# Kernel optimization log

Hardware: AMD Instinct MI355X
Metric: run time of the kernel (lower is better)

Reference implementation:

```python
import math
import jax, jax.numpy as jnp
import numpy as np

B, T, D, H, FACTOR = 8, 4096, 1024, 16, 5
DH = D // H


def setup_inputs() -> dict:
    key = jax.random.key(0)
    ks = jax.random.split(key, 7)
    u = max(1, min(int(FACTOR * math.log(T + 1)), T))  # = 41
    s = 1.0 / np.sqrt(D).astype(np.float32)
    x = jax.random.normal(ks[0], (B, T, D), jnp.float32)
    Wq = jax.random.normal(ks[1], (D, D), jnp.float32) * s
    Wk = jax.random.normal(ks[2], (D, D), jnp.float32) * s
    Wv = jax.random.normal(ks[3], (D, D), jnp.float32) * s
    Wo = jax.random.normal(ks[4], (D, D), jnp.float32) * s
    bo = jax.random.normal(ks[5], (D,), jnp.float32) * 0.01
    # unique indices, mirroring torch.randperm(T)[:u]
    idx = jax.random.permutation(ks[6], T)[:u].astype(jnp.int32)
    return {"x": x, "Wq": Wq, "Wk": Wk, "Wv": Wv, "Wo": Wo, "bo": bo, "idx": idx}


def reference(x, Wq, Wk, Wv, Wo, bo, idx):
    Bx, Tx, Dx = x.shape
    scale = 1.0 / np.sqrt(DH).astype(np.float32)

    def proj(W):  # torch Linear: x @ W.T, then split heads -> [B,H,T,Dh]
        return (x @ W.T).reshape(Bx, Tx, H, DH).transpose(0, 2, 1, 3)

    Q = proj(Wq)
    K = proj(Wk)
    V = proj(Wv)

    Qs = Q[:, :, idx, :]                                   # [B,H,u,Dh] gather
    scores = jnp.einsum('bhud,bhtd->bhut', Qs, K) * scale  # [B,H,u,T]
    attn = jax.nn.softmax(scores, axis=-1)
    ctx = jnp.einsum('bhut,bhtd->bhud', attn, V)           # [B,H,u,Dh]

    # mean over the u sampled positions fills non-sampled slots
    out = jnp.broadcast_to(ctx.mean(axis=2, keepdims=True), (Bx, H, Tx, DH))
    out = out.at[:, :, idx, :].set(ctx)                    # scatter ctx back

    y = out.transpose(0, 2, 1, 3).reshape(Bx, Tx, Dx)
    return y @ Wo.T + bo
```

## Files before the change

kernel.cpp:

```cpp
#include <hip/hip_runtime.h>
#include <hip/hip_bf16.h>

#define B_  8
#define T_  4096
#define D_  1024
#define H_  16
#define DH_ 64
#define NC_ 4

typedef __bf16 bf8 __attribute__((ext_vector_type(8)));
typedef float f32x4 __attribute__((ext_vector_type(4)));

__device__ __forceinline__ unsigned short f2bf_rn(float f) {
    unsigned u = __float_as_uint(f);
    unsigned r = (u + 0x7FFF + ((u >> 16) & 1)) >> 16;
    return (unsigned short)r;
}

__device__ __forceinline__ void async_load16(const void* gp, void* lp) {
    __builtin_amdgcn_global_load_lds(
        (const __attribute__((address_space(1))) unsigned*)(gp),
        (__attribute__((address_space(3))) unsigned*)(lp), 16, 0, 0);
}


__global__ void k_sel(const int* __restrict__ idx, int* __restrict__ sel, int U) {
    for (int t = threadIdx.x; t < T_; t += 256) sel[t] = 0;
    __syncthreads();
    if (threadIdx.x < U) sel[idx[threadIdx.x]] = threadIdx.x + 1;
}

__global__ void k_gather(const float* __restrict__ x, const int* __restrict__ idx,
                         float* __restrict__ xs, int U) {
    int bi = blockIdx.x;
    int b = bi / U, i = bi - b * U;
    int t = idx[i];
    const float4* src = (const float4*)(x + ((size_t)(b * T_ + t)) * D_);
    float4* dst = (float4*)(xs + (size_t)bi * D_);
    dst[threadIdx.x] = src[threadIdx.x];
}

__global__ void k_cvt_flat(const float* __restrict__ src, short* __restrict__ dst) {
    size_t i = ((size_t)blockIdx.x * 256 + threadIdx.x) * 8;
    float4 a = *(const float4*)(src + i);
    float4 b = *(const float4*)(src + i + 4);
    short4 s0, s1;
    s0.x = (short)f2bf_rn(a.x); s0.y = (short)f2bf_rn(a.y);
    s0.z = (short)f2bf_rn(a.z); s0.w = (short)f2bf_rn(a.w);
    s1.x = (short)f2bf_rn(b.x); s1.y = (short)f2bf_rn(b.y);
    s1.z = (short)f2bf_rn(b.z); s1.w = (short)f2bf_rn(b.w);
    *(short4*)(dst + i) = s0;
    *(short4*)(dst + i + 4) = s1;
}

__global__ __launch_bounds__(256) void k_proj(const float* __restrict__ A,
                                              const float* __restrict__ W,
                                              const float* __restrict__ bias,
                                              float* __restrict__ C, int M) {
    __shared__ float As[32][64 + 4];
    __shared__ float Bs[32][64 + 4];
    int m0 = blockIdx.x * 64, n0 = blockIdx.y * 64;
    int tid = threadIdx.x;
    int lr = tid >> 3;
    int lc = (tid & 7) * 4;
    int ty = tid >> 4, tx = tid & 15;
    float acc[4][4] = {{0.f}};
    for (int k0 = 0; k0 < D_; k0 += 32) {
#pragma unroll
        for (int half = 0; half < 2; ++half) {
            int r = lr + half * 32;
            int gm = m0 + r;
            float4 v = make_float4(0.f, 0.f, 0.f, 0.f);
            if (gm < M) v = *(const float4*)(A + (size_t)gm * D_ + k0 + lc);
            As[lc + 0][r] = v.x; As[lc + 1][r] = v.y; As[lc + 2][r] = v.z; As[lc + 3][r] = v.w;
            int gn = n0 + r;
            float4 w = *(const float4*)(W + (size_t)gn * D_ + k0 + lc);
            Bs[lc + 0][r] = w.x; Bs[lc + 1][r] = w.y; Bs[lc + 2][r] = w.z; Bs[lc + 3][r] = w.w;
        }
        __syncthreads();
#pragma unroll
        for (int kk = 0; kk < 32; ++kk) {
            float4 a = *(const float4*)&As[kk][ty * 4];
            float4 bb = *(const float4*)&Bs[kk][tx * 4];
            acc[0][0] += a.x * bb.x; acc[0][1] += a.x * bb.y; acc[0][2] += a.x * bb.z; acc[0][3] += a.x * bb.w;
            acc[1][0] += a.y * bb.x; acc[1][1] += a.y * bb.y; acc[1][2] += a.y * bb.z; acc[1][3] += a.y * bb.w;
            acc[2][0] += a.z * bb.x; acc[2][1] += a.z * bb.y; acc[2][2] += a.z * bb.z; acc[2][3] += a.z * bb.w;
            acc[3][0] += a.w * bb.x; acc[3][1] += a.w * bb.y; acc[3][2] += a.w * bb.z; acc[3][3] += a.w * bb.w;
        }
        __syncthreads();
    }
#pragma unroll
    for (int i = 0; i < 4; ++i) {
        int gm = m0 + ty * 4 + i;
        if (gm < M) {
            int gn = n0 + tx * 4;
            float4 v = make_float4(acc[i][0], acc[i][1], acc[i][2], acc[i][3]);
            if (bias) {
                v.x += bias[gn + 0]; v.y += bias[gn + 1];
                v.z += bias[gn + 2]; v.w += bias[gn + 3];
            }
            *(float4*)(C + (size_t)gm * D_ + gn) = v;
        }
    }
}

__global__ __launch_bounds__(256) void k_qth(const float* __restrict__ Qs,
                                             const float* __restrict__ Wk,
                                             short* __restrict__ Qtb, int U, int MP) {
    __shared__ float As[32][64 + 4];
    __shared__ float Bs[32][64 + 4];
    int h = blockIdx.z;
    int m0 = blockIdx.x * 64, n0 = blockIdx.y * 64;
    int BU = B_ * U;
    int tid = threadIdx.x;
    int lr = tid >> 3, lc = (tid & 7) * 4;
    int ty = tid >> 4, tx = tid & 15;
    float acc[4][4] = {{0.f}};
    for (int k0 = 0; k0 < DH_; k0 += 32) {
#pragma unroll
        for (int half = 0; half < 2; ++half) {
            int r = lr + half * 32;
            int gm = m0 + r;
            float4 v = make_float4(0.f, 0.f, 0.f, 0.f);
            if (gm < BU) v = *(const float4*)(Qs + (size_t)gm * D_ + h * DH_ + k0 + lc);
            As[lc + 0][r] = v.x; As[lc + 1][r] = v.y; As[lc + 2][r] = v.z; As[lc + 3][r] = v.w;
            int kr = (tid >> 4) + half * 16;
            int nc = (tid & 15) * 4;
            float4 w = *(const float4*)(Wk + ((size_t)(h * DH_ + k0 + kr)) * D_ + n0 + nc);
            *(float4*)&Bs[kr][nc] = w;
        }
        __syncthreads();
#pragma unroll
        for (int kk = 0; kk < 32; ++kk) {
            float4 a = *(const float4*)&As[kk][ty * 4];
            float4 bb = *(const float4*)&Bs[kk][tx * 4];
            acc[0][0] += a.x * bb.x; acc[0][1] += a.x * bb.y; acc[0][2] += a.x * bb.z; acc[0][3] += a.x * bb.w;
            acc[1][0] += a.y * bb.x; acc[1][1] += a.y * bb.y; acc[1][2] += a.y * bb.z; acc[1][3] += a.y * bb.w;
            acc[2][0] += a.z * bb.x; acc[2][1] += a.z * bb.y; acc[2][2] += a.z * bb.z; acc[2][3] += a.z * bb.w;
            acc[3][0] += a.w * bb.x; acc[3][1] += a.w * bb.y; acc[3][2] += a.w * bb.z; acc[3][3] += a.w * bb.w;
        }
        __syncthreads();
    }
#pragma unroll
    for (int i = 0; i < 4; ++i) {
        int gm = m0 + ty * 4 + i;
        if (gm < BU) {
            int b = gm / U, ii = gm - b * U;
            short4 s;
            s.x = (short)f2bf_rn(0.125f * acc[i][0]);
            s.y = (short)f2bf_rn(0.125f * acc[i][1]);
            s.z = (short)f2bf_rn(0.125f * acc[i][2]);
            s.w = (short)f2bf_rn(0.125f * acc[i][3]);
            *(short4*)(Qtb + ((size_t)b * MP + h * U + ii) * D_ + n0 + tx * 4) = s;
        }
    }
}

#define GEMM_NT 16

__device__ __forceinline__ void stage64(const short* __restrict__ Ag,
                                        const short* __restrict__ Bg,
                                        short* lA, short* lB, int kt, int tid) {
#pragma unroll
    for (int i = 0; i < 4; ++i) {
        int li = i * 512 + tid;
        int row = li >> 3, sl = li & 7;
        int off = row * D_ + kt + ((sl ^ (row & 7)) << 3);
        async_load16(Ag + off, lA + li * 8);
        async_load16(Bg + off, lB + li * 8);
    }
}

__device__ __forceinline__ bf8 lds_frag(const short* l, int R, int slot) {
    return *(const bf8*)(l + R * 64 + (((slot) ^ (R & 7)) << 3));
}

__device__ __forceinline__ void gemm256_core(const short* __restrict__ Ag,
                                             const short* __restrict__ Bg,
                                             short* lA0, short* lB0,
                                             f32x4 (&acc)[8][4]) {
    int tid = threadIdx.x;
    int lane = tid & 63, w = tid >> 6;
    int wr = w >> 2, wc = w & 3;
    int ln = lane & 15, q = lane >> 4;
#pragma unroll
    for (int mi = 0; mi < 8; ++mi)
#pragma unroll
        for (int ni = 0; ni < 4; ++ni)
            acc[mi][ni] = (f32x4){0.f, 0.f, 0.f, 0.f};

    stage64(Ag, Bg, lA0, lB0, 0, tid);
    stage64(Ag, Bg, lA0 + 16384, lB0 + 16384, 64, tid);

#pragma unroll 1
    for (int t = 0; t < GEMM_NT; ++t) {
        const int p = t & 1;
        short* lA = lA0 + p * 16384;
        short* lB = lB0 + p * 16384;
        if (t < GEMM_NT - 1) asm volatile("s_waitcnt vmcnt(8)" ::: "memory");
        else                 asm volatile("s_waitcnt vmcnt(0)" ::: "memory");
        __builtin_amdgcn_s_barrier();

        bf8 bfrag[4][2], afrag[4][2];
#pragma unroll
        for (int ni = 0; ni < 4; ++ni)
#pragma unroll
            for (int kh = 0; kh < 2; ++kh)
                bfrag[ni][kh] = lds_frag(lB, wc * 64 + ni * 16 + ln, kh * 4 + q);
#pragma unroll
        for (int mi = 0; mi < 4; ++mi)
#pragma unroll
            for (int kh = 0; kh < 2; ++kh)
                afrag[mi][kh] = lds_frag(lA, wr * 128 + mi * 16 + ln, kh * 4 + q);
        __builtin_amdgcn_s_setprio(1);
#pragma unroll
        for (int kh = 0; kh < 2; ++kh)
#pragma unroll
            for (int mi = 0; mi < 4; ++mi)
#pragma unroll
                for (int ni = 0; ni < 4; ++ni)
                    acc[mi][ni] = __builtin_amdgcn_mfma_f32_16x16x32_bf16(
                        afrag[mi][kh], bfrag[ni][kh], acc[mi][ni], 0, 0, 0);
        __builtin_amdgcn_s_setprio(0);
#pragma unroll
        for (int mi = 0; mi < 4; ++mi)
#pragma unroll
            for (int kh = 0; kh < 2; ++kh)
                afrag[mi][kh] = lds_frag(lA, wr * 128 + 64 + mi * 16 + ln, kh * 4 + q);
        __builtin_amdgcn_s_setprio(1);
#pragma unroll
        for (int kh = 0; kh < 2; ++kh)
#pragma unroll
            for (int mi = 0; mi < 4; ++mi)
#pragma unroll
                for (int ni = 0; ni < 4; ++ni)
                    acc[4 + mi][ni] = __builtin_amdgcn_mfma_f32_16x16x32_bf16(
                        afrag[mi][kh], bfrag[ni][kh], acc[4 + mi][ni], 0, 0, 0);
        __builtin_amdgcn_s_setprio(0);
        asm volatile("" ::: "memory");
        __builtin_amdgcn_s_barrier();
        if (t + 2 < GEMM_NT)
            stage64(Ag, Bg, lA, lB, (t + 2) * 64, tid);
    }
}

__global__ __launch_bounds__(512, 2) void k_gemm(const short* __restrict__ Qtb,
                                                 const short* __restrict__ xb,
                                                 const short* __restrict__ Wvb,
                                                 short* __restrict__ attnb,
                                                 short* __restrict__ Vt, int MP) {
    __shared__ short lAB[4][16384];
    int bid = blockIdx.x;
    int cpx = gridDim.x >> 3;
    int lg = (bid & 7) * cpx + (bid >> 3);
    int tid = threadIdx.x;
    int lane = tid & 63, w = tid >> 6;
    int wr = w >> 2, wc = w & 3;
    int ln = lane & 15, q = lane >> 4;
    f32x4 acc[8][4];

    if (lg < 512) {
        int mt = lg >> 2, nt = lg & 3;
        gemm256_core(xb + (size_t)mt * 256 * D_, Wvb + (size_t)nt * 256 * D_,
                     &lAB[0][0], &lAB[2][0], acc);
        int h = nt * 4 + wc;
        int b = mt >> 4;
        int tIn = (mt & 15) * 256 + wr * 128;
        const int PITCH = 136;
        short* ep = &lAB[0][0] + w * 2304;
        size_t vbase = ((size_t)(b * H_ + h) * DH_) * T_;
#pragma unroll
        for (int ni = 0; ni < 4; ++ni) {
#pragma unroll
            for (int mi = 0; mi < 8; ++mi) {
                short4 s;
                s.x = (short)f2bf_rn(acc[mi][ni][0]);
                s.y = (short)f2bf_rn(acc[mi][ni][1]);
                s.z = (short)f2bf_rn(acc[mi][ni][2]);
                s.w = (short)f2bf_rn(acc[mi][ni][3]);
                *(short4*)(ep + ln * PITCH + mi * 16 + q * 4) = s;
            }
            __syncthreads();
#pragma unroll
            for (int it = 0; it < 2; ++it) {
                int dhl = it * 8 + (lane >> 3);
                int seg = lane & 7;
                bf8 v0 = *(const bf8*)(ep + dhl * PITCH + seg * 8);
                bf8 v1 = *(const bf8*)(ep + dhl * PITCH + (seg + 8) * 8);
                int dh = ni * 16 + dhl;
                *(bf8*)(Vt + vbase + (size_t)dh * T_ + tIn + seg * 8) = v0;
                *(bf8*)(Vt + vbase + (size_t)dh * T_ + tIn + 64 + seg * 8) = v1;
            }
            __syncthreads();
        }
    } else {
        int r2 = lg - 512;
        int b = r2 / 48;
        int rr = r2 - b * 48;
        int mt = rr >> 4, nt = rr & 15;
        gemm256_core(Qtb + ((size_t)b * MP + mt * 256) * D_,
                     xb + ((size_t)b * T_ + nt * 256) * D_,
                     &lAB[0][0], &lAB[2][0], acc);
        short* Cb = attnb + (size_t)b * MP * T_;
        int row0 = mt * 256 + wr * 128;
        int col0 = nt * 256 + wc * 64;
#pragma unroll
        for (int mi = 0; mi < 8; ++mi)
#pragma unroll
            for (int ni = 0; ni < 4; ++ni) {
                int col = col0 + ni * 16 + ln;
#pragma unroll
                for (int rr2 = 0; rr2 < 4; ++rr2) {
                    int grow = row0 + mi * 16 + q * 4 + rr2;
                    Cb[(size_t)grow * T_ + col] = (short)f2bf_rn(__expf(acc[mi][ni][rr2]));
                }
            }
    }
}

__global__ __launch_bounds__(256) void k_pv(const short* __restrict__ attnb,
                                            const short* __restrict__ Vt,
                                            float* __restrict__ Op,
                                            float* __restrict__ rsp,
                                            int U, int MP) {
    __shared__ short vt[64 * 136];
    __shared__ short at[48 * 136];
    int gid = blockIdx.x;
    int c = gid & (NC_ - 1);
    int bh = gid >> 2;
    int h = bh & (H_ - 1);
    int b = bh >> 4;
    int tid = threadIdx.x;
    int lane = tid & 63, w = tid >> 6;
    int quad = lane >> 4;
    const short* Arow = attnb + ((size_t)b * MP + h * U) * T_;
    const short* Vrow = Vt + (size_t)bh * DH_ * T_;

    f32x4 O[3];
#pragma unroll
    for (int mi = 0; mi < 3; ++mi) O[mi] = (f32x4){0.f, 0.f, 0.f, 0.f};
    float rs[3] = {0.f, 0.f, 0.f};

    for (int tt = 0; tt < (T_ / NC_) / 128; ++tt) {
        int t0 = c * (T_ / NC_) + tt * 128;
#pragma unroll
        for (int it = 0; it < 4; ++it) {
            int idx = it * 256 + tid;
            int dh = idx >> 4, seg = idx & 15;
            bf8 v = *(const bf8*)(Vrow + (size_t)dh * T_ + t0 + seg * 8);
            *(bf8*)(vt + dh * 136 + seg * 8) = v;
        }
#pragma unroll
        for (int it = 0; it < 3; ++it) {
            int idx = it * 256 + tid;
            int r = idx >> 4, seg = idx & 15;
            bf8 v = *(const bf8*)(Arow + (size_t)r * T_ + t0 + seg * 8);
            *(bf8*)(at + r * 136 + seg * 8) = v;
        }
        __syncthreads();
        bf8 af[3][4];
#pragma unroll
        for (int mi = 0; mi < 3; ++mi)
#pragma unroll
            for (int kf = 0; kf < 4; ++kf)
                af[mi][kf] = *(const bf8*)(at + (mi * 16 + (lane & 15)) * 136 + kf * 32 + quad * 8);
        if (w == 0) {
#pragma unroll
            for (int mi = 0; mi < 3; ++mi)
#pragma unroll
                for (int kf = 0; kf < 4; ++kf)
#pragma unroll
                    for (int j = 0; j < 8; ++j) rs[mi] += (float)af[mi][kf][j];
        }
#pragma unroll
        for (int kf = 0; kf < 4; ++kf) {
            bf8 bfr = *(const bf8*)(vt + (w * 16 + (lane & 15)) * 136 + kf * 32 + quad * 8);
#pragma unroll
            for (int mi = 0; mi < 3; ++mi)
                O[mi] = __builtin_amdgcn_mfma_f32_16x16x32_bf16(af[mi][kf], bfr, O[mi], 0, 0, 0);
        }
        __syncthreads();
    }
#pragma unroll
    for (int mi = 0; mi < 3; ++mi)
#pragma unroll
        for (int r = 0; r < 4; ++r)
            Op[((size_t)gid * 48 + mi * 16 + quad * 4 + r) * DH_ + w * 16 + (lane & 15)] = O[mi][r];
    if (w == 0) {
#pragma unroll
        for (int mi = 0; mi < 3; ++mi) {
            rs[mi] += __shfl_xor(rs[mi], 16);
            rs[mi] += __shfl_xor(rs[mi], 32);
            if (quad == 0) rsp[(size_t)gid * 48 + mi * 16 + lane] = rs[mi];
        }
    }
}

__global__ __launch_bounds__(256) void k_rows2(const float* __restrict__ Op,
                                               const float* __restrict__ rsp,
                                               float* __restrict__ R, int U) {
    __shared__ float inv[48];
    __shared__ float msum[4][64];
    int bh = blockIdx.x;
    int b = bh >> 4, h = bh & (H_ - 1);
    int tid = threadIdx.x;
    if (tid < 48) {
        float s = 0.f;
        for (int cc = 0; cc < NC_; ++cc) s += rsp[(size_t)(bh * NC_ + cc) * 48 + tid];
        inv[tid] = 1.f / s;
    }
    __syncthreads();
    int dh = tid & 63, ig = tid >> 6;
    float acc = 0.f;
    for (int p = 0; p < 11; ++p) {
        int i = p * 4 + ig;
        if (i < U) {
            float o = 0.f;
            for (int cc = 0; cc < NC_; ++cc)
                o += Op[((size_t)(bh * NC_ + cc) * 48 + i) * DH_ + dh];
            float v = o * inv[i];
            R[((size_t)b * (U + 1) + 1 + i) * D_ + h * DH_ + dh] = v;
            acc += v;
        }
    }
    msum[ig][dh] = acc;
    __syncthreads();
    if (ig == 0)
        R[((size_t)b * (U + 1)) * D_ + h * DH_ + dh] =
            (msum[0][dh] + msum[1][dh] + msum[2][dh] + msum[3][dh]) / (float)U;
}

__global__ __launch_bounds__(256) void k_fill(const float* __restrict__ Yr,
                                              const int* __restrict__ sel,
                                              float* __restrict__ y, int U) {
    int blk = blockIdx.x;
    int b = blk >> 12, t = blk & (T_ - 1);
    int j = sel[t];
    const float4* src = (const float4*)(Yr + ((size_t)b * (U + 1) + j) * D_);
    float4* dst = (float4*)(y + (size_t)blk * D_);
    dst[threadIdx.x] = src[threadIdx.x];
}

extern "C" void kernel_launch(void* const* d_in, const int* in_sizes, int n_in,
                              void* d_out, int out_size, void* d_ws, size_t ws_size,
                              hipStream_t stream) {
    const float* x  = (const float*)d_in[0];
    const float* Wq = (const float*)d_in[1];
    const float* Wk = (const float*)d_in[2];
    const float* Wv = (const float*)d_in[3];
    const float* Wo = (const float*)d_in[4];
    const float* bo = (const float*)d_in[5];
    const int*  idx = (const int*)d_in[6];
    int U = in_sizes[6];
    int HU = H_ * U;
    int MP = ((HU + 127) / 128) * 128;

    char* w = (char*)d_ws;
    auto alloc = [&](size_t bytes) { char* p = w; w += (bytes + 255) & ~(size_t)255; return p; };

    float* xs    = (float*)alloc((size_t)B_ * U * D_ * 4);
    float* Qs    = (float*)alloc((size_t)B_ * U * D_ * 4);
    short* Qtb   = (short*)alloc((size_t)B_ * MP * D_ * 2);
    short* xb    = (short*)alloc((size_t)B_ * T_ * D_ * 2);
    short* Wvb   = (short*)alloc((size_t)D_ * D_ * 2);
    short* attnb = (short*)alloc((size_t)B_ * MP * T_ * 2);
    short* Vtb   = (short*)alloc((size_t)B_ * D_ * T_ * 2);
    float* Opb   = (float*)alloc((size_t)B_ * H_ * NC_ * 48 * DH_ * 4);
    float* rspb  = (float*)alloc((size_t)B_ * H_ * NC_ * 48 * 4);
    float* R     = (float*)alloc((size_t)B_ * (U + 1) * D_ * 4);
    float* Yr    = (float*)alloc((size_t)B_ * (U + 1) * D_ * 4);
    int*   sel   = (int*)alloc((size_t)T_ * 4);

    k_sel<<<dim3(1), dim3(256), 0, stream>>>(idx, sel, U);
    k_gather<<<dim3(B_ * U), dim3(256), 0, stream>>>(x, idx, xs, U);
    k_proj<<<dim3((B_ * U + 63) / 64, D_ / 64), dim3(256), 0, stream>>>(xs, Wq, nullptr, Qs, B_ * U);
    k_cvt_flat<<<dim3((size_t)B_ * T_ * D_ / 2048), dim3(256), 0, stream>>>(x, xb);
    k_cvt_flat<<<dim3((size_t)D_ * D_ / 2048), dim3(256), 0, stream>>>(Wv, Wvb);
    k_qth<<<dim3((B_ * U + 63) / 64, D_ / 64, H_), dim3(256), 0, stream>>>(Qs, Wk, Qtb, U, MP);
    k_gemm<<<dim3(512 + B_ * 48), dim3(512), 0, stream>>>(Qtb, xb, Wvb, attnb, Vtb, MP);
    k_pv<<<dim3(B_ * H_ * NC_), dim3(256), 0, stream>>>(attnb, Vtb, Opb, rspb, U, MP);
    k_rows2<<<dim3(B_ * H_), dim3(256), 0, stream>>>(Opb, rspb, R, U);
    k_proj<<<dim3((B_ * (U + 1) + 63) / 64, D_ / 64), dim3(256), 0, stream>>>(R, Wo, bo, Yr, B_ * (U + 1));
    k_fill<<<dim3(B_ * T_), dim3(256), 0, stream>>>(Yr, sel, (float*)d_out, U);
}
```

Measured before the change: 566.8 us.

## Shrink fused GEMM tiles to 128x128 with K=32 stages and merge conversion kernels

Replaces the 256x256 tile, 512-thread GEMM core with a 128x128 tile, 256-thread core that stages K in 32-wide double-buffered LDS chunks. The V-projection and score epilogues are rewritten to match the smaller tiles. The grid grows from 896 to 3584 blocks to improve occupancy and load balance. The two fp32-to-bf16 conversion launches are also merged into one kernel, saving a launch, at the cost of lower per-tile data reuse and more global loads.

```diff
diff --git a/kernel.cpp b/kernel.cpp
--- a/kernel.cpp
+++ b/kernel.cpp
@@ -40,15 +40,21 @@
     dst[threadIdx.x] = src[threadIdx.x];
 }
 
-__global__ void k_cvt_flat(const float* __restrict__ src, short* __restrict__ dst) {
-    size_t i = ((size_t)blockIdx.x * 256 + threadIdx.x) * 8;
-    float4 a = *(const float4*)(src + i);
-    float4 b = *(const float4*)(src + i + 4);
+__global__ void k_cvt2(const float* __restrict__ a, const float* __restrict__ bsrc,
+                       short* __restrict__ da, short* __restrict__ db, int n1) {
+    int blk = blockIdx.x;
+    const float* src;
+    short* dst;
+    size_t i;
+    if (blk < n1) { src = a;    dst = da; i = ((size_t)blk * 256 + threadIdx.x) * 8; }
+    else          { src = bsrc; dst = db; i = ((size_t)(blk - n1) * 256 + threadIdx.x) * 8; }
+    float4 va = *(const float4*)(src + i);
+    float4 vb = *(const float4*)(src + i + 4);
     short4 s0, s1;
-    s0.x = (short)f2bf_rn(a.x); s0.y = (short)f2bf_rn(a.y);
-    s0.z = (short)f2bf_rn(a.z); s0.w = (short)f2bf_rn(a.w);
-    s1.x = (short)f2bf_rn(b.x); s1.y = (short)f2bf_rn(b.y);
-    s1.z = (short)f2bf_rn(b.z); s1.w = (short)f2bf_rn(b.w);
+    s0.x = (short)f2bf_rn(va.x); s0.y = (short)f2bf_rn(va.y);
+    s0.z = (short)f2bf_rn(va.z); s0.w = (short)f2bf_rn(va.w);
+    s1.x = (short)f2bf_rn(vb.x); s1.y = (short)f2bf_rn(vb.y);
+    s1.z = (short)f2bf_rn(vb.z); s1.w = (short)f2bf_rn(vb.w);
     *(short4*)(dst + i) = s0;
     *(short4*)(dst + i + 4) = s1;
 }
@@ -156,123 +162,106 @@
     }
 }
 
-#define GEMM_NT 16
-
-__device__ __forceinline__ void stage64(const short* __restrict__ Ag,
+#define NT32 (D_ / 32)
+
+__device__ __forceinline__ void stage32(const short* __restrict__ Ag,
                                         const short* __restrict__ Bg,
                                         short* lA, short* lB, int kt, int tid) {
 #pragma unroll
-    for (int i = 0; i < 4; ++i) {
-        int li = i * 512 + tid;
-        int row = li >> 3, sl = li & 7;
-        int off = row * D_ + kt + ((sl ^ (row & 7)) << 3);
+    for (int i = 0; i < 2; ++i) {
+        int li = i * 256 + tid;
+        int row = li >> 2, sl = li & 3;
+        int off = row * D_ + kt + ((sl ^ (row & 3)) << 3);
         async_load16(Ag + off, lA + li * 8);
+    }
+#pragma unroll
+    for (int i = 0; i < 2; ++i) {
+        int li = i * 256 + tid;
+        int row = li >> 2, sl = li & 3;
+        int off = row * D_ + kt + ((sl ^ (row & 3)) << 3);
         async_load16(Bg + off, lB + li * 8);
     }
 }
 
-__device__ __forceinline__ bf8 lds_frag(const short* l, int R, int slot) {
-    return *(const bf8*)(l + R * 64 + (((slot) ^ (R & 7)) << 3));
-}
-
-__device__ __forceinline__ void gemm256_core(const short* __restrict__ Ag,
+__device__ __forceinline__ bf8 lds_frag32(const short* l, int R, int q) {
+    return *(const bf8*)(l + R * 32 + ((q ^ (R & 3)) << 3));
+}
+
+__device__ __forceinline__ void gemm128_core(const short* __restrict__ Ag,
                                              const short* __restrict__ Bg,
-                                             short* lA0, short* lB0,
-                                             f32x4 (&acc)[8][4]) {
+                                             short* sm, f32x4 (&acc)[4][4]) {
     int tid = threadIdx.x;
     int lane = tid & 63, w = tid >> 6;
-    int wr = w >> 2, wc = w & 3;
+    int wr = w >> 1, wc = w & 1;
     int ln = lane & 15, q = lane >> 4;
-#pragma unroll
-    for (int mi = 0; mi < 8; ++mi)
+    short* lA0 = sm;
+    short* lB0 = sm + 8192;
+#pragma unroll
+    for (int mi = 0; mi < 4; ++mi)
 #pragma unroll
         for (int ni = 0; ni < 4; ++ni)
             acc[mi][ni] = (f32x4){0.f, 0.f, 0.f, 0.f};
 
-    stage64(Ag, Bg, lA0, lB0, 0, tid);
-    stage64(Ag, Bg, lA0 + 16384, lB0 + 16384, 64, tid);
+    stage32(Ag, Bg, lA0, lB0, 0, tid);
+    stage32(Ag, Bg, lA0 + 4096, lB0 + 4096, 32, tid);
 
 #pragma unroll 1
-    for (int t = 0; t < GEMM_NT; ++t) {
+    for (int t = 0; t < NT32; ++t) {
         const int p = t & 1;
-        short* lA = lA0 + p * 16384;
-        short* lB = lB0 + p * 16384;
-        if (t < GEMM_NT - 1) asm volatile("s_waitcnt vmcnt(8)" ::: "memory");
-        else                 asm volatile("s_waitcnt vmcnt(0)" ::: "memory");
+        const short* lA = lA0 + p * 4096;
+        const short* lB = lB0 + p * 4096;
+        if (t < NT32 - 1) asm volatile("s_waitcnt vmcnt(4)" ::: "memory");
+        else              asm volatile("s_waitcnt vmcnt(0)" ::: "memory");
         __builtin_amdgcn_s_barrier();
 
-        bf8 bfrag[4][2], afrag[4][2];
-#pragma unroll
-        for (int ni = 0; ni < 4; ++ni)
-#pragma unroll
-            for (int kh = 0; kh < 2; ++kh)
-                bfrag[ni][kh] = lds_frag(lB, wc * 64 + ni * 16 + ln, kh * 4 + q);
+        bf8 af[4], bf[4];
+#pragma unroll
+        for (int ni = 0; ni < 4; ++ni) bf[ni] = lds_frag32(lB, wc * 64 + ni * 16 + ln, q);
+#pragma unroll
+        for (int mi = 0; mi < 4; ++mi) af[mi] = lds_frag32(lA, wr * 64 + mi * 16 + ln, q);
+        __builtin_amdgcn_s_setprio(1);
 #pragma unroll
         for (int mi = 0; mi < 4; ++mi)
 #pragma unroll
-            for (int kh = 0; kh < 2; ++kh)
-                afrag[mi][kh] = lds_frag(lA, wr * 128 + mi * 16 + ln, kh * 4 + q);
-        __builtin_amdgcn_s_setprio(1);
-#pragma unroll
-        for (int kh = 0; kh < 2; ++kh)
-#pragma unroll
-            for (int mi = 0; mi < 4; ++mi)
-#pragma unroll
-                for (int ni = 0; ni < 4; ++ni)
-                    acc[mi][ni] = __builtin_amdgcn_mfma_f32_16x16x32_bf16(
-                        afrag[mi][kh], bfrag[ni][kh], acc[mi][ni], 0, 0, 0);
-        __builtin_amdgcn_s_setprio(0);
-#pragma unroll
-        for (int mi = 0; mi < 4; ++mi)
-#pragma unroll
-            for (int kh = 0; kh < 2; ++kh)
-                afrag[mi][kh] = lds_frag(lA, wr * 128 + 64 + mi * 16 + ln, kh * 4 + q);
-        __builtin_amdgcn_s_setprio(1);
-#pragma unroll
-        for (int kh = 0; kh < 2; ++kh)
-#pragma unroll
-            for (int mi = 0; mi < 4; ++mi)
-#pragma unroll
-                for (int ni = 0; ni < 4; ++ni)
-                    acc[4 + mi][ni] = __builtin_amdgcn_mfma_f32_16x16x32_bf16(
-                        afrag[mi][kh], bfrag[ni][kh], acc[4 + mi][ni], 0, 0, 0);
+            for (int ni = 0; ni < 4; ++ni)
+                acc[mi][ni] = __builtin_amdgcn_mfma_f32_16x16x32_bf16(
+                    af[mi], bf[ni], acc[mi][ni], 0, 0, 0);
         __builtin_amdgcn_s_setprio(0);
         asm volatile("" ::: "memory");
         __builtin_amdgcn_s_barrier();
-        if (t + 2 < GEMM_NT)
-            stage64(Ag, Bg, lA, lB, (t + 2) * 64, tid);
-    }
-}
-
-__global__ __launch_bounds__(512, 2) void k_gemm(const short* __restrict__ Qtb,
+        if (t + 2 < NT32)
+            stage32(Ag, Bg, lA0 + p * 4096, lB0 + p * 4096, (t + 2) * 32, tid);
+    }
+}
+
+__global__ __launch_bounds__(256, 2) void k_gemm(const short* __restrict__ Qtb,
                                                  const short* __restrict__ xb,
                                                  const short* __restrict__ Wvb,
                                                  short* __restrict__ attnb,
                                                  short* __restrict__ Vt, int MP) {
-    __shared__ short lAB[4][16384];
+    __shared__ short sm[16384];
     int bid = blockIdx.x;
     int cpx = gridDim.x >> 3;
     int lg = (bid & 7) * cpx + (bid >> 3);
     int tid = threadIdx.x;
     int lane = tid & 63, w = tid >> 6;
-    int wr = w >> 2, wc = w & 3;
+    int wr = w >> 1, wc = w & 1;
     int ln = lane & 15, q = lane >> 4;
-    f32x4 acc[8][4];
-
-    if (lg < 512) {
-        int mt = lg >> 2, nt = lg & 3;
-        gemm256_core(xb + (size_t)mt * 256 * D_, Wvb + (size_t)nt * 256 * D_,
-                     &lAB[0][0], &lAB[2][0], acc);
-        int h = nt * 4 + wc;
-        int b = mt >> 4;
-        int tIn = (mt & 15) * 256 + wr * 128;
-        const int PITCH = 136;
-        short* ep = &lAB[0][0] + w * 2304;
+    f32x4 acc[4][4];
+
+    if (lg < 2048) {
+        int mt = lg >> 3, nt = lg & 7;
+        gemm128_core(xb + (size_t)mt * 128 * D_, Wvb + (size_t)nt * 128 * D_, sm, acc);
+        int h = nt * 2 + wc;
+        int b = mt >> 5;
+        int tIn = (mt & 31) * 128 + wr * 64;
+        const int PITCH = 72;
+        short* ep = sm + w * 1152;
         size_t vbase = ((size_t)(b * H_ + h) * DH_) * T_;
 #pragma unroll
         for (int ni = 0; ni < 4; ++ni) {
 #pragma unroll
-            for (int mi = 0; mi < 8; ++mi) {
+            for (int mi = 0; mi < 4; ++mi) {
                 short4 s;
                 s.x = (short)f2bf_rn(acc[mi][ni][0]);
                 s.y = (short)f2bf_rn(acc[mi][ni][1]);
@@ -285,27 +274,24 @@
             for (int it = 0; it < 2; ++it) {
                 int dhl = it * 8 + (lane >> 3);
                 int seg = lane & 7;
-                bf8 v0 = *(const bf8*)(ep + dhl * PITCH + seg * 8);
-                bf8 v1 = *(const bf8*)(ep + dhl * PITCH + (seg + 8) * 8);
+                bf8 v = *(const bf8*)(ep + dhl * PITCH + seg * 8);
                 int dh = ni * 16 + dhl;
-                *(bf8*)(Vt + vbase + (size_t)dh * T_ + tIn + seg * 8) = v0;
-                *(bf8*)(Vt + vbase + (size_t)dh * T_ + tIn + 64 + seg * 8) = v1;
+                *(bf8*)(Vt + vbase + (size_t)dh * T_ + tIn + seg * 8) = v;
             }
             __syncthreads();
         }
     } else {
-        int r2 = lg - 512;
-        int b = r2 / 48;
-        int rr = r2 - b * 48;
-        int mt = rr >> 4, nt = rr & 15;
-        gemm256_core(Qtb + ((size_t)b * MP + mt * 256) * D_,
-                     xb + ((size_t)b * T_ + nt * 256) * D_,
-                     &lAB[0][0], &lAB[2][0], acc);
+        int r2 = lg - 2048;
+        int b = r2 / 192;
+        int rr = r2 - b * 192;
+        int mt = rr >> 5, nt = rr & 31;
+        gemm128_core(Qtb + ((size_t)b * MP + mt * 128) * D_,
+                     xb + ((size_t)b * T_ + nt * 128) * D_, sm, acc);
         short* Cb = attnb + (size_t)b * MP * T_;
-        int row0 = mt * 256 + wr * 128;
-        int col0 = nt * 256 + wc * 64;
-#pragma unroll
-        for (int mi = 0; mi < 8; ++mi)
+        int row0 = mt * 128 + wr * 64;
+        int col0 = nt * 128 + wc * 64;
+#pragma unroll
+        for (int mi = 0; mi < 4; ++mi)
 #pragma unroll
             for (int ni = 0; ni < 4; ++ni) {
                 int col = col0 + ni * 16 + ln;
@@ -471,13 +457,15 @@
     float* Yr    = (float*)alloc((size_t)B_ * (U + 1) * D_ * 4);
     int*   sel   = (int*)alloc((size_t)T_ * 4);
 
+    int n1 = (int)((size_t)B_ * T_ * D_ / 2048);
+    int n2 = (int)((size_t)D_ * D_ / 2048);
+
     k_sel<<<dim3(1), dim3(256), 0, stream>>>(idx, sel, U);
     k_gather<<<dim3(B_ * U), dim3(256), 0, stream>>>(x, idx, xs, U);
     k_proj<<<dim3((B_ * U + 63) / 64, D_ / 64), dim3(256), 0, stream>>>(xs, Wq, nullptr, Qs, B_ * U);
-    k_cvt_flat<<<dim3((size_t)B_ * T_ * D_ / 2048), dim3(256), 0, stream>>>(x, xb);
-    k_cvt_flat<<<dim3((size_t)D_ * D_ / 2048), dim3(256), 0, stream>>>(Wv, Wvb);
+    k_cvt2<<<dim3(n1 + n2), dim3(256), 0, stream>>>(x, Wv, xb, Wvb, n1);
     k_qth<<<dim3((B_ * U + 63) / 64, D_ / 64, H_), dim3(256), 0, stream>>>(Qs, Wk, Qtb, U, MP);
-    k_gemm<<<dim3(512 + B_ * 48), dim3(512), 0, stream>>>(Qtb, xb, Wvb, attnb, Vtb, MP);
+    k_gemm<<<dim3(2048 + B_ * 192), dim3(256), 0, stream>>>(Qtb, xb, Wvb, attnb, Vtb, MP);
     k_pv<<<dim3(B_ * H_ * NC_), dim3(256), 0, stream>>>(attnb, Vtb, Opb, rspb, U, MP);
     k_rows2<<<dim3(B_ * H_), dim3(256), 0, stream>>>(Opb, rspb, R, U);
     k_proj<<<dim3((B_ * (U + 1) + 63) / 64, D_ / 64), dim3(256), 0, stream>>>(R, Wo, bo, Yr, B_ * (U + 1));
```

Result: slower. 588.4 us (+3.8%).
